# Performance work log

Measured on AMD Instinct MI355X. Metric: run time of the kernel, lower is better.

The kernel has to match this reference:

```python
import jax, jax.numpy as jnp
import numpy as np

HIDDEN = 256
NUM_LEVELS = 4
BATCH = 256
NUM_SLOTS = 64
NUM_FEATURES = 4096


def setup_inputs() -> dict:
    key = jax.random.key(0)
    ks = jax.random.split(key, 6)
    s = 1.0 / np.sqrt(HIDDEN)
    return {
        "attention_weights": jax.random.uniform(ks[0], (BATCH, NUM_SLOTS, NUM_FEATURES), dtype=jnp.float32),
        "current_centers": jax.random.normal(ks[1], (NUM_FEATURES, HIDDEN), dtype=jnp.float32),
        "w_ih": jax.random.uniform(ks[2], (3 * HIDDEN, HIDDEN), jnp.float32, -s, s),
        "w_hh": jax.random.uniform(ks[3], (3 * HIDDEN, HIDDEN), jnp.float32, -s, s),
        "b_ih": jax.random.uniform(ks[4], (3 * HIDDEN,), jnp.float32, -s, s),
        "b_hh": jax.random.uniform(ks[5], (3 * HIDDEN,), jnp.float32, -s, s),
        "num_levels": NUM_LEVELS,
    }


def reference(attention_weights, current_centers, w_ih, w_hh, b_ih, b_hh, num_levels):
    B, S, F = attention_weights.shape
    H = current_centers.shape[1]
    O = S // num_levels  # num_objects

    # aggregated features: bmm with shared center matrix -> [B, S, H]
    x = jnp.einsum("bsf,fh->bsh", attention_weights, current_centers)

    # per-slot hidden state: slot i*L+j uses current_centers[i] -> [S, H]
    h = jnp.repeat(current_centers[:O], num_levels, axis=0)

    # fused GRUCell gates over all (batch, slot) pairs (torch gate order: r, z, n)
    gi = x @ w_ih.T + b_ih            # [B, S, 3H]
    gh = h @ w_hh.T + b_hh            # [S, 3H], broadcasts over batch
    gi_r, gi_z, gi_n = jnp.split(gi, 3, axis=-1)
    gh_r, gh_z, gh_n = jnp.split(gh, 3, axis=-1)

    r = jax.nn.sigmoid(gi_r + gh_r)
    z = jax.nn.sigmoid(gi_z + gh_z)
    n = jnp.tanh(gi_n + r * gh_n)
    h_new = (1.0 - z) * n + z * h     # [B, S, H]

    # average the num_levels updates per object, then stack objects first
    out = h_new.reshape(B, O, num_levels, H).mean(axis=2)  # [B, O, H]
    return jnp.transpose(out, (1, 0, 2))                   # [O, B, H]
```

## Files before the change

kernel.cpp:

```cpp
#include <hip/hip_runtime.h>
#include <stdint.h>


typedef _Float16 half8 __attribute__((ext_vector_type(8)));
typedef float f32x4 __attribute__((ext_vector_type(4)));

#define WS_CT   0u
#define WS_WP   2097152u
#define WS_GH   2490368u
#define WS_CSP  2686976u
#define WS_CS   2752512u
#define WS_CSW  2753536u
#define WS_X    2756608u

static __device__ __forceinline__ _Float16 f2h(float x) {
  return (_Float16)x;
}
static __device__ __forceinline__ void gload16(const void* g, void* lds) {
  __builtin_amdgcn_global_load_lds(
      (const __attribute__((address_space(1))) unsigned int*)g,
      (__attribute__((address_space(3))) unsigned int*)lds, 16, 0, 0);
}
static __device__ __forceinline__ float sigmf(float x) {
  float e = __expf(-fabsf(x));
  float p = 1.f / (1.f + e);
  return x >= 0.f ? p : 1.f - p;
}
static __device__ __forceinline__ float tanhf2(float x) {
  float e = __expf(-2.f * fabsf(x));
  float t = 1.f - 2.f * e / (1.f + e);
  return x >= 0.f ? t : -t;
}

__global__ void __launch_bounds__(256) k_transC(const float* __restrict__ C,
                                                _Float16* __restrict__ Ct) {
  __shared__ float sT[64][65];
  const int f0 = blockIdx.x * 64, h0 = blockIdx.y * 64;
  const int t = threadIdx.x;
#pragma unroll
  for (int i = 0; i < 4; ++i) {
    int fl = t + 256 * i;
    int r = fl >> 4, c4 = fl & 15;
    float4 v = *(const float4*)(C + (size_t)(f0 + r) * 256 + h0 + c4 * 4);
    sT[r][c4 * 4 + 0] = v.x; sT[r][c4 * 4 + 1] = v.y;
    sT[r][c4 * 4 + 2] = v.z; sT[r][c4 * 4 + 3] = v.w;
  }
  __syncthreads();
#pragma unroll
  for (int i = 0; i < 2; ++i) {
    int q = t + 256 * i;
    int hr = q >> 3, j = q & 7;
    int h = h0 + hr;
    union { half8 v; _Float16 u[8]; } pk;
#pragma unroll
    for (int u = 0; u < 8; ++u) pk.u[u] = f2h(sT[j * 8 + u][hr]);
    size_t off = (size_t)h * 8192 + (size_t)f0 * 2 + (size_t)((j ^ (h & 7)) << 4);
    *(half8*)((char*)Ct + off) = pk.v;
  }
}

__global__ void __launch_bounds__(256) k_csum(const float* __restrict__ C,
                                              float* __restrict__ part) {
  const int b = blockIdx.x, t = threadIdx.x;
  float s = 0.f;
  for (int k = 0; k < 64; ++k) s += C[(size_t)(b * 64 + k) * 256 + t];
  part[b * 256 + t] = s;
}
__global__ void __launch_bounds__(256) k_csum2(const float* __restrict__ part,
                                               float* __restrict__ csum) {
  const int t = threadIdx.x;
  float s = 0.f;
#pragma unroll
  for (int b = 0; b < 64; ++b) s += part[b * 256 + t];
  csum[t] = 0.5f * s;
}
__global__ void __launch_bounds__(256) k_csumW(const float* __restrict__ w_ih,
                                               const float* __restrict__ cs,
                                               float* __restrict__ csW) {
  const int wv = threadIdx.x >> 6, l = threadIdx.x & 63;
  const int n = blockIdx.x * 4 + wv;
  float4 w = *(const float4*)(w_ih + (size_t)n * 256 + l * 4);
  float4 c = *(const float4*)(cs + l * 4);
  float s = w.x * c.x + w.y * c.y + w.z * c.z + w.w * c.w;
#pragma unroll
  for (int off = 32; off; off >>= 1) s += __shfl_down(s, off, 64);
  if (l == 0) csW[n] = s;
}

__global__ void __launch_bounds__(256) k_prepWp(const float* __restrict__ w_ih,
                                                _Float16* __restrict__ Wp) {
  int q = blockIdx.x * 256 + threadIdx.x;
  int row = q >> 5, c = q & 31;
  int seg = c >> 3, j = c & 7;
  int srow = (row % 3) * 256 + row / 3;
  const float* src = w_ih + (size_t)srow * 256 + c * 8;
  union { half8 v; _Float16 u[8]; } pk;
#pragma unroll
  for (int u = 0; u < 8; ++u) pk.u[u] = f2h(src[u]);
  size_t off = (size_t)row * 512 + seg * 128 + ((j ^ (row & 7)) << 4);
  *(half8*)((char*)Wp + off) = pk.v;
}

__global__ void __launch_bounds__(256) k_gh(const float* __restrict__ centers,
                                            const float* __restrict__ w_hh,
                                            const float* __restrict__ b_hh,
                                            float* __restrict__ GH) {
  __shared__ __align__(16) float sH[256];
  const int s = blockIdx.x, t = threadIdx.x;
  sH[t] = centers[(size_t)(s >> 2) * 256 + t];
  __syncthreads();
#pragma unroll
  for (int e = 0; e < 3; ++e) {
    int n = e * 256 + t;
    float accv = b_hh[n];
    const float4* w = (const float4*)(w_hh + (size_t)n * 256);
#pragma unroll 8
    for (int k = 0; k < 64; ++k) {
      float4 v = w[k];
      float4 hh = *(const float4*)&sH[k * 4];
      accv += v.x * hh.x + v.y * hh.y + v.z * hh.z + v.w * hh.w;
    }
    GH[(size_t)s * 768 + n] = accv;
  }
}

__global__ void __launch_bounds__(256, 2) k_stage1(const float* __restrict__ A,
                                                   const _Float16* __restrict__ Ct,
                                                   _Float16* __restrict__ X) {
  __shared__ __align__(16) _Float16 sA0[32 * 64];
  __shared__ __align__(16) _Float16 sA1[32 * 64];
  __shared__ __align__(16) _Float16 sB0[256 * 64];
  __shared__ __align__(16) _Float16 sB1[256 * 64];
  const int t = threadIdx.x;
  const int wid = t >> 6, l = t & 63;
  const int lr = l & 15, lk = l >> 4;
  const int m0 = blockIdx.x * 32;

  f32x4 acc[2][4];
#pragma unroll
  for (int i = 0; i < 2; ++i)
#pragma unroll
    for (int j = 0; j < 4; ++j) acc[i][j] = (f32x4){0.f, 0.f, 0.f, 0.f};

  const int ar = t >> 3, aj = t & 7;
  const float* aptr = A + (size_t)(m0 + ar) * 4096 + aj * 8;
  const int saw = ar * 128 + ((aj ^ (ar & 7)) << 4);

  const int br = t >> 3, bj = t & 7;

  f32x4 aEv[2], aOd[2];

#pragma unroll
  for (int i = 0; i < 8; ++i)
    gload16(Ct + (size_t)(br + 32 * i) * 4096 + bj * 8,
            (char*)sB0 + (wid * 64 + 256 * i) * 16);
  aEv[0] = __builtin_nontemporal_load((const f32x4*)(aptr));
  aEv[1] = __builtin_nontemporal_load((const f32x4*)(aptr + 4));
  aOd[0] = __builtin_nontemporal_load((const f32x4*)(aptr + 64));
  aOd[1] = __builtin_nontemporal_load((const f32x4*)(aptr + 64 + 4));
  {
    union { half8 v; _Float16 u[8]; } pk;
    pk.u[0] = f2h(aEv[0].x - 0.5f); pk.u[1] = f2h(aEv[0].y - 0.5f);
    pk.u[2] = f2h(aEv[0].z - 0.5f); pk.u[3] = f2h(aEv[0].w - 0.5f);
    pk.u[4] = f2h(aEv[1].x - 0.5f); pk.u[5] = f2h(aEv[1].y - 0.5f);
    pk.u[6] = f2h(aEv[1].z - 0.5f); pk.u[7] = f2h(aEv[1].w - 0.5f);
    *(half8*)((char*)sA0 + saw) = pk.v;
  }

  auto body = [&](int kk, const _Float16* sAc, const _Float16* sBc,
                  _Float16* sAn, _Float16* sBn, f32x4* aWr, f32x4* aLd) {
    if (kk == 63) {
      asm volatile("s_waitcnt vmcnt(0)" ::: "memory");
    } else {
      asm volatile("s_waitcnt vmcnt(2)" ::: "memory");
    }
    asm volatile("s_waitcnt lgkmcnt(0)" ::: "memory");
    __builtin_amdgcn_s_barrier();
    __builtin_amdgcn_sched_barrier(0);
    if (kk <= 62) {
#pragma unroll
      for (int i = 0; i < 8; ++i)
        gload16(Ct + (size_t)(br + 32 * i) * 4096 + (size_t)(kk + 1) * 64 + bj * 8,
                (char*)sBn + (wid * 64 + 256 * i) * 16);
    }
    if (kk <= 61) {
      const float* ap = aptr + (kk + 2) * 64;
      aLd[0] = __builtin_nontemporal_load((const f32x4*)(ap));
      aLd[1] = __builtin_nontemporal_load((const f32x4*)(ap + 4));
    }
    if (kk <= 62) {
      union { half8 v; _Float16 u[8]; } pk;
      pk.u[0] = f2h(aWr[0].x - 0.5f); pk.u[1] = f2h(aWr[0].y - 0.5f);
      pk.u[2] = f2h(aWr[0].z - 0.5f); pk.u[3] = f2h(aWr[0].w - 0.5f);
      pk.u[4] = f2h(aWr[1].x - 0.5f); pk.u[5] = f2h(aWr[1].y - 0.5f);
      pk.u[6] = f2h(aWr[1].z - 0.5f); pk.u[7] = f2h(aWr[1].w - 0.5f);
      *(half8*)((char*)sAn + saw) = pk.v;
    }
#pragma unroll
    for (int kc = 0; kc < 2; ++kc) {
      const int q = kc * 4 + lk;
      half8 af[2], bf[4];
#pragma unroll
      for (int mi = 0; mi < 2; ++mi) {
        int rl = mi * 16 + lr;
        af[mi] = *(const half8*)((const char*)sAc + rl * 128 + ((q ^ (rl & 7)) << 4));
      }
#pragma unroll
      for (int ni = 0; ni < 4; ++ni) {
        int rb = wid * 64 + ni * 16 + lr;
        bf[ni] = *(const half8*)((const char*)sBc + rb * 128 + ((q ^ (rb & 7)) << 4));
      }
#pragma unroll
      for (int mi = 0; mi < 2; ++mi)
#pragma unroll
        for (int ni = 0; ni < 4; ++ni)
          acc[mi][ni] = __builtin_amdgcn_mfma_f32_16x16x32_f16(af[mi], bf[ni], acc[mi][ni], 0, 0, 0);
    }
  };

  for (int kx = 0; kx < 64; kx += 2) {
    body(kx + 0, sA0, sB0, sA1, sB1, aOd, aEv);
    body(kx + 1, sA1, sB1, sA0, sB0, aEv, aOd);
  }

#pragma unroll
  for (int mi = 0; mi < 2; ++mi)
#pragma unroll
    for (int ni = 0; ni < 4; ++ni)
#pragma unroll
      for (int p = 0; p < 4; ++p) {
        int m = m0 + mi * 16 + lk * 4 + p;
        int col = wid * 64 + ni * 16 + lr;
        size_t off = (size_t)m * 512 + ((col >> 6) << 7) +
                     ((((col >> 3) & 7) ^ (m & 7)) << 4) + ((col & 7) << 1);
        *(_Float16*)((char*)X + off) = f2h(acc[mi][ni][p]);
      }
}

__global__ void __launch_bounds__(256) k_stage2(const _Float16* __restrict__ X,
                                                const _Float16* __restrict__ Wp,
                                                const float* __restrict__ GH,
                                                const float* __restrict__ centers,
                                                const float* __restrict__ b_ih,
                                                const float* __restrict__ csW,
                                                float* __restrict__ out) {
  __shared__ __align__(16) char smem[81920];
  _Float16* sX = (_Float16*)smem;
  char*     sW = smem + 32768;
  float*    sC = (float*)(smem + 32768);
  const int t = threadIdx.x;
  const int wid = t >> 6, l = t & 63;
  const int lr = l & 15, lk = l >> 4;
  const int wm = wid >> 1, wn = wid & 1;
  const int b = blockIdx.x;

#pragma unroll
  for (int i = 0; i < 8; ++i) {
    int flat = t + 256 * i;
    gload16((const char*)X + ((size_t)b * 64 + (flat >> 5)) * 512 +
                (size_t)(flat & 31) * 16,
            (char*)sX + (wid * 64 + 256 * i) * 16);
  }
  __syncthreads();

  for (int nt = 0; nt < 8; ++nt) {
    const int n0 = nt * 96;
    f32x4 acc[2][3];
#pragma unroll
    for (int i = 0; i < 2; ++i)
#pragma unroll
      for (int j = 0; j < 3; ++j) acc[i][j] = (f32x4){0.f, 0.f, 0.f, 0.f};

#pragma unroll
    for (int i = 0; i < 12; ++i) {
      int flat = t + 256 * i;
      gload16((const char*)Wp + (size_t)(n0 + (flat >> 5)) * 512 +
                  (size_t)(flat & 31) * 16,
              sW + (wid * 64 + 256 * i) * 16);
    }
    __syncthreads();
#pragma unroll
    for (int kc = 0; kc < 8; ++kc) {
      const int q = kc * 4 + lk;
      const int seg = (q >> 3) << 7, jj = q & 7;
      half8 af[2];
#pragma unroll
      for (int mi = 0; mi < 2; ++mi) {
        int rl = wm * 32 + mi * 16 + lr;
        af[mi] = *(const half8*)((const char*)sX + rl * 512 + seg + ((jj ^ (rl & 7)) << 4));
      }
#pragma unroll
      for (int ni = 0; ni < 3; ++ni) {
        int rw = wn * 48 + ni * 16 + lr;
        half8 bf = *(const half8*)(sW + rw * 512 + seg + ((jj ^ (rw & 7)) << 4));
#pragma unroll
        for (int mi = 0; mi < 2; ++mi)
          acc[mi][ni] = __builtin_amdgcn_mfma_f32_16x16x32_f16(af[mi], bf, acc[mi][ni], 0, 0, 0);
      }
    }
    __syncthreads();
#pragma unroll
    for (int mi = 0; mi < 2; ++mi)
#pragma unroll
      for (int ni = 0; ni < 3; ++ni)
#pragma unroll
        for (int p = 0; p < 4; ++p) {
          int row = wm * 32 + mi * 16 + lk * 4 + p;
          int col = wn * 48 + ni * 16 + lr;
          sC[row * 100 + col] = acc[mi][ni][p];
        }
    __syncthreads();
#pragma unroll
    for (int ii = 0; ii < 2; ++ii) {
      int item = t + 256 * ii;
      int hl = item & 31, o = item >> 5;
      int h = nt * 32 + hl;
      float hprev = centers[o * 256 + h];
      float bir = b_ih[h] + csW[h];
      float biz = b_ih[256 + h] + csW[256 + h];
      float bin = b_ih[512 + h] + csW[512 + h];
      float sum = 0.f;
#pragma unroll
      for (int j = 0; j < 4; ++j) {
        int s = 4 * o + j;
        float gir = sC[s * 100 + 3 * hl + 0] + bir;
        float giz = sC[s * 100 + 3 * hl + 1] + biz;
        float gin = sC[s * 100 + 3 * hl + 2] + bin;
        float rg = sigmf(gir + GH[s * 768 + h]);
        float zg = sigmf(giz + GH[s * 768 + 256 + h]);
        float ng = tanhf2(gin + rg * GH[s * 768 + 512 + h]);
        sum += (1.f - zg) * ng + zg * hprev;
      }
      out[(size_t)o * 65536 + (size_t)b * 256 + h] = 0.25f * sum;
    }
    __syncthreads();
  }
}

extern "C" void kernel_launch(void* const* d_in, const int* in_sizes, int n_in,
                              void* d_out, int out_size, void* d_ws, size_t ws_size,
                              hipStream_t stream) {
  (void)in_sizes; (void)n_in; (void)out_size; (void)ws_size;
  const float* attn    = (const float*)d_in[0];
  const float* centers = (const float*)d_in[1];
  const float* w_ih    = (const float*)d_in[2];
  const float* w_hh    = (const float*)d_in[3];
  const float* b_ih    = (const float*)d_in[4];
  const float* b_hh    = (const float*)d_in[5];

  char* ws = (char*)d_ws;
  _Float16* Ct  = (_Float16*)(ws + WS_CT);
  _Float16* Wpp = (_Float16*)(ws + WS_WP);
  float*    GHp = (float*)(ws + WS_GH);
  float*    csp = (float*)(ws + WS_CSP);
  float*    cs  = (float*)(ws + WS_CS);
  float*    csW = (float*)(ws + WS_CSW);
  _Float16* X   = (_Float16*)(ws + WS_X);
  float* out = (float*)d_out;

  hipLaunchKernelGGL(k_transC, dim3(64, 4), dim3(256), 0, stream, centers, Ct);
  hipLaunchKernelGGL(k_csum, dim3(64), dim3(256), 0, stream, centers, csp);
  hipLaunchKernelGGL(k_csum2, dim3(1), dim3(256), 0, stream, csp, cs);
  hipLaunchKernelGGL(k_csumW, dim3(192), dim3(256), 0, stream, w_ih, cs, csW);
  hipLaunchKernelGGL(k_prepWp, dim3(96), dim3(256), 0, stream, w_ih, Wpp);
  hipLaunchKernelGGL(k_gh, dim3(64), dim3(256), 0, stream, centers, w_hh, b_hh, GHp);
  hipLaunchKernelGGL(k_stage1, dim3(512), dim3(256), 0, stream, attn, Ct, X);
  hipLaunchKernelGGL(k_stage2, dim3(256), dim3(256), 0, stream, X, Wpp, GHp, centers, b_ih, csW, out);
}
```

Measured before the change: 167.4 us.

## Load A fragments straight from global into registers, bypassing LDS staging

Stage 1 stops staging the fp32 attention matrix through shared memory. Each lane now loads its MFMA A-fragment directly from global memory into registers one tile ahead, and converts it to fp16 just before the MFMA. This removes the A LDS writes and reads and the lgkmcnt wait, and frees LDS. In exchange, all four waves fetch the same A rows redundantly, the nontemporal hint is dropped, prefetch distance shrinks from two tiles to one, and register use rises.

```diff
diff --git a/kernel.cpp b/kernel.cpp
--- a/kernel.cpp
+++ b/kernel.cpp
@@ -127,8 +127,6 @@
 __global__ void __launch_bounds__(256, 2) k_stage1(const float* __restrict__ A,
                                                    const _Float16* __restrict__ Ct,
                                                    _Float16* __restrict__ X) {
-  __shared__ __align__(16) _Float16 sA0[32 * 64];
-  __shared__ __align__(16) _Float16 sA1[32 * 64];
   __shared__ __align__(16) _Float16 sB0[256 * 64];
   __shared__ __align__(16) _Float16 sB1[256 * 64];
   const int t = threadIdx.x;
@@ -142,39 +140,30 @@
 #pragma unroll
     for (int j = 0; j < 4; ++j) acc[i][j] = (f32x4){0.f, 0.f, 0.f, 0.f};
 
-  const int ar = t >> 3, aj = t & 7;
-  const float* aptr = A + (size_t)(m0 + ar) * 4096 + aj * 8;
-  const int saw = ar * 128 + ((aj ^ (ar & 7)) << 4);
-
   const int br = t >> 3, bj = t & 7;
 
-  f32x4 aEv[2], aOd[2];
+  const float* aBase = A + (size_t)(m0 + lr) * 4096 + lk * 8;
+
+  f32x4 aP[4][2], aQ[4][2];
 
 #pragma unroll
   for (int i = 0; i < 8; ++i)
     gload16(Ct + (size_t)(br + 32 * i) * 4096 + bj * 8,
             (char*)sB0 + (wid * 64 + 256 * i) * 16);
-  aEv[0] = __builtin_nontemporal_load((const f32x4*)(aptr));
-  aEv[1] = __builtin_nontemporal_load((const f32x4*)(aptr + 4));
-  aOd[0] = __builtin_nontemporal_load((const f32x4*)(aptr + 64));
-  aOd[1] = __builtin_nontemporal_load((const f32x4*)(aptr + 64 + 4));
-  {
-    union { half8 v; _Float16 u[8]; } pk;
-    pk.u[0] = f2h(aEv[0].x - 0.5f); pk.u[1] = f2h(aEv[0].y - 0.5f);
-    pk.u[2] = f2h(aEv[0].z - 0.5f); pk.u[3] = f2h(aEv[0].w - 0.5f);
-    pk.u[4] = f2h(aEv[1].x - 0.5f); pk.u[5] = f2h(aEv[1].y - 0.5f);
-    pk.u[6] = f2h(aEv[1].z - 0.5f); pk.u[7] = f2h(aEv[1].w - 0.5f);
-    *(half8*)((char*)sA0 + saw) = pk.v;
-  }
-
-  auto body = [&](int kk, const _Float16* sAc, const _Float16* sBc,
-                  _Float16* sAn, _Float16* sBn, f32x4* aWr, f32x4* aLd) {
-    if (kk == 63) {
-      asm volatile("s_waitcnt vmcnt(0)" ::: "memory");
-    } else {
-      asm volatile("s_waitcnt vmcnt(2)" ::: "memory");
-    }
-    asm volatile("s_waitcnt lgkmcnt(0)" ::: "memory");
+  __builtin_amdgcn_sched_barrier(0);
+#pragma unroll
+  for (int mi = 0; mi < 2; ++mi)
+#pragma unroll
+    for (int kc = 0; kc < 2; ++kc) {
+      const float* p = aBase + (size_t)mi * 16 * 4096 + kc * 32;
+      aP[mi * 2 + kc][0] = *(const f32x4*)p;
+      aP[mi * 2 + kc][1] = *(const f32x4*)(p + 4);
+    }
+  __builtin_amdgcn_sched_barrier(0);
+
+  auto body = [&](int kk, const _Float16* sBc, _Float16* sBn,
+                  f32x4 (&aC)[4][2], f32x4 (&aN)[4][2]) {
+    asm volatile("s_waitcnt vmcnt(8)" ::: "memory");
     __builtin_amdgcn_s_barrier();
     __builtin_amdgcn_sched_barrier(0);
     if (kk <= 62) {
@@ -183,27 +172,33 @@
         gload16(Ct + (size_t)(br + 32 * i) * 4096 + (size_t)(kk + 1) * 64 + bj * 8,
                 (char*)sBn + (wid * 64 + 256 * i) * 16);
     }
-    if (kk <= 61) {
-      const float* ap = aptr + (kk + 2) * 64;
-      aLd[0] = __builtin_nontemporal_load((const f32x4*)(ap));
-      aLd[1] = __builtin_nontemporal_load((const f32x4*)(ap + 4));
-    }
+    __builtin_amdgcn_sched_barrier(0);
     if (kk <= 62) {
-      union { half8 v; _Float16 u[8]; } pk;
-      pk.u[0] = f2h(aWr[0].x - 0.5f); pk.u[1] = f2h(aWr[0].y - 0.5f);
-      pk.u[2] = f2h(aWr[0].z - 0.5f); pk.u[3] = f2h(aWr[0].w - 0.5f);
-      pk.u[4] = f2h(aWr[1].x - 0.5f); pk.u[5] = f2h(aWr[1].y - 0.5f);
-      pk.u[6] = f2h(aWr[1].z - 0.5f); pk.u[7] = f2h(aWr[1].w - 0.5f);
-      *(half8*)((char*)sAn + saw) = pk.v;
-    }
+      const float* ap = aBase + (size_t)(kk + 1) * 64;
+#pragma unroll
+      for (int mi = 0; mi < 2; ++mi)
+#pragma unroll
+        for (int kc = 0; kc < 2; ++kc) {
+          const float* p = ap + (size_t)mi * 16 * 4096 + kc * 32;
+          aN[mi * 2 + kc][0] = *(const f32x4*)p;
+          aN[mi * 2 + kc][1] = *(const f32x4*)(p + 4);
+        }
+    }
+    __builtin_amdgcn_sched_barrier(0);
 #pragma unroll
     for (int kc = 0; kc < 2; ++kc) {
       const int q = kc * 4 + lk;
       half8 af[2], bf[4];
 #pragma unroll
       for (int mi = 0; mi < 2; ++mi) {
-        int rl = mi * 16 + lr;
-        af[mi] = *(const half8*)((const char*)sAc + rl * 128 + ((q ^ (rl & 7)) << 4));
+        union { half8 v; _Float16 u[8]; } pk;
+        const f32x4 x0 = aC[mi * 2 + kc][0];
+        const f32x4 x1 = aC[mi * 2 + kc][1];
+        pk.u[0] = f2h(x0.x - 0.5f); pk.u[1] = f2h(x0.y - 0.5f);
+        pk.u[2] = f2h(x0.z - 0.5f); pk.u[3] = f2h(x0.w - 0.5f);
+        pk.u[4] = f2h(x1.x - 0.5f); pk.u[5] = f2h(x1.y - 0.5f);
+        pk.u[6] = f2h(x1.z - 0.5f); pk.u[7] = f2h(x1.w - 0.5f);
+        af[mi] = pk.v;
       }
 #pragma unroll
       for (int ni = 0; ni < 4; ++ni) {
@@ -219,8 +214,8 @@
   };
 
   for (int kx = 0; kx < 64; kx += 2) {
-    body(kx + 0, sA0, sB0, sA1, sB1, aOd, aEv);
-    body(kx + 1, sA1, sB1, sA0, sB0, aEv, aOd);
+    body(kx + 0, sB0, sB1, aP, aQ);
+    body(kx + 1, sB1, sB0, aQ, aP);
   }
 
 #pragma unroll
```

After: 249.2 us. 1.49x slower.
